# Kernel optimization log

Measured on AMD Instinct MI355X. Metric: run time of the kernel, lower is better.

Reference implementation:

```python
import jax, jax.numpy as jnp
import numpy as np

B, CIN, COUT, K = 4096, 128, 128, 9  # batch, in_ch, out_ch, board size / n_offsets


def setup_inputs() -> dict:
    key = jax.random.key(0)
    k1, k2, k3 = jax.random.split(key, 3)
    inputs = jax.random.normal(k1, (B, CIN, K, K), dtype=jnp.float32)   # [B, Cin, 9, 9]
    weights = jax.random.normal(k2, (K, COUT, CIN), dtype=jnp.float32)  # per-offset linear
    bias = jax.random.normal(k3, (K, COUT), dtype=jnp.float32)
    return {"inputs": inputs, "weights": weights, "bias": bias}


def reference(inputs, weights, bias):
    # For each vertical offset k (row of the 9x9 board), gather the slice
    # inputs[:, :, k, :] and apply the k-th linear map plus its bias.
    # out[b, k, oc, x] = sum_i W[k, oc, i] * inputs[b, i, k, x] + bias[k, oc]
    out = jnp.einsum('bikx,koi->bkox', inputs, weights)  # [B, 9, Cout, 9]
    out = out + bias[None, :, :, None]
    return out
```

## Files before the change

kernel.cpp:

```cpp
#include <hip/hip_runtime.h>
#include <hip/hip_bf16.h>


#define NB    4096
#define CINC  128
#define COUTC 128
#define NK    9
#define NX    9
#define BT    4
#define NCOL  (BT * NX)
#define LDK   136
#define ROWF  (NK * NX)
#define OUTK  (COUTC * NX)
#define OUTB  (NK * OUTK)
#define NWELT (NK * COUTC * CINC)

typedef __attribute__((ext_vector_type(8))) short short8;
typedef __attribute__((ext_vector_type(4))) float floatx4;

struct F4 { float x, y, z, w; };

__device__ __forceinline__ short f2bf(float f) {
    union { float f; unsigned u; } v; v.f = f;
    unsigned r = v.u + 0x7fff + ((v.u >> 16) & 1);
    return (short)(r >> 16);
}

__global__ __launch_bounds__(256) void GatherVertical_40656160424516_wconv(
    const float* __restrict__ w, short* __restrict__ wbf)
{
    int idx = blockIdx.x * 256 + threadIdx.x;
    wbf[idx] = f2bf(w[idx]);
}

__global__ __launch_bounds__(512, 8) void GatherVertical_40656160424516_kernel(
    const float* __restrict__ in, const short* __restrict__ wbf,
    const float* __restrict__ bias, float* __restrict__ out)
{
    __shared__ __align__(16) char smem[NCOL * LDK * 2 + BT * OUTK * 4];
    short* Il = (short*)smem;
    float* Ol = (float*)(smem + NCOL * LDK * 2);

    const int t = threadIdx.x;
    const int b0 = blockIdx.x * BT;

    const int lane = t & 63;
    const int wv = t >> 6;
    const int lc = lane & 15;
    const int quad = lane >> 4;
    const int oc_base = wv * 16;

    const int i_st = t & 127;
    const int bl_st = t >> 7;
    const float* rowp = in + ((size_t)(b0 + bl_st) * CINC + i_st) * ROWF;

    F4 sa, sb; float sc;
    auto issue_in = [&](int k) {
        const float* p = rowp + k * NX;
        sa = *(const F4*)p; sb = *(const F4*)(p + 4); sc = p[8];
    };
    issue_in(0);

    short* Ilb = Il + bl_st * (NX * LDK) + i_st;

    for (int k = 0; k < NK; ++k) {
        Ilb[0 * LDK] = f2bf(sa.x);
        Ilb[1 * LDK] = f2bf(sa.y);
        Ilb[2 * LDK] = f2bf(sa.z);
        Ilb[3 * LDK] = f2bf(sa.w);
        Ilb[4 * LDK] = f2bf(sb.x);
        Ilb[5 * LDK] = f2bf(sb.y);
        Ilb[6 * LDK] = f2bf(sb.z);
        Ilb[7 * LDK] = f2bf(sb.w);
        Ilb[8 * LDK] = f2bf(sc);

        asm volatile("s_waitcnt lgkmcnt(0)" ::: "memory");
        __builtin_amdgcn_s_barrier();

        const short* wpk = wbf + k * (COUTC * CINC) + (oc_base + lc) * CINC + quad * 8;
        short8 afr[4];
        #pragma unroll
        for (int s = 0; s < 4; ++s) afr[s] = *(const short8*)(wpk + s * 32);
        float4 bv = *(const float4*)(bias + k * COUTC + oc_base + quad * 4);
        __builtin_amdgcn_sched_barrier(0);
        if (k < NK - 1) issue_in(k + 1);
        __builtin_amdgcn_sched_barrier(0);

        float bsv[4] = {bv.x, bv.y, bv.z, bv.w};

        floatx4 acc[3];
        #pragma unroll
        for (int n = 0; n < 3; ++n) acc[n] = (floatx4){0.f, 0.f, 0.f, 0.f};
        #pragma unroll
        for (int s = 0; s < 4; ++s) {
            const int kof = s * 32 + quad * 8;
            #pragma unroll
            for (int n = 0; n < 3; ++n) {
                const int col = (n < 2) ? (n * 16 + lc) : (32 + (lc & 3));
                short8 bfr = *(const short8*)&Il[col * LDK + kof];
                acc[n] = __builtin_amdgcn_mfma_f32_16x16x32_bf16(afr[s], bfr, acc[n], 0, 0, 0);
            }
        }

        #pragma unroll
        for (int n = 0; n < 2; ++n) {
            int nx = n * 16 + lc;
            int bl = nx / 9;
            int x = nx - bl * 9;
            float* op = Ol + (bl * COUTC + oc_base + quad * 4) * NX + x;
            #pragma unroll
            for (int r = 0; r < 4; ++r) op[r * NX] = acc[n][r] + bsv[r];
        }
        if (lc < 4) {
            float* op = Ol + (3 * COUTC + oc_base + quad * 4) * NX + 5 + lc;
            #pragma unroll
            for (int r = 0; r < 4; ++r) op[r * NX] = acc[2][r] + bsv[r];
        }

        asm volatile("s_waitcnt lgkmcnt(0)" ::: "memory");
        __builtin_amdgcn_s_barrier();

        float* dstk = out + (size_t)b0 * OUTB + k * OUTK;
        #pragma unroll
        for (int c = 0; c < 2; ++c) {
            int fo = (c * 512 + t) * 4;
            int bl = fo / 1152;
            int rem = fo - bl * 1152;
            floatx4 v = *(const floatx4*)(Ol + fo);
            *(floatx4*)(dstk + (size_t)bl * OUTB + rem) = v;
        }
        if (t < 128) {
            int fo = (1024 + t) * 4;
            int rem = fo - 3 * 1152;
            floatx4 v = *(const floatx4*)(Ol + fo);
            *(floatx4*)(dstk + (size_t)3 * OUTB + rem) = v;
        }
    }
}

__global__ __launch_bounds__(512, 4) void GatherVertical_40656160424516_fb(
    const float* __restrict__ in, const float* __restrict__ w,
    const float* __restrict__ bias, float* __restrict__ out)
{
    __shared__ __align__(16) char smem[NCOL * LDK * 2 + BT * OUTK * 4];
    short* Il = (short*)smem;
    float* Ol = (float*)(smem + NCOL * LDK * 2);

    const int t = threadIdx.x;
    const int b0 = blockIdx.x * BT;
    const int lane = t & 63;
    const int wv = t >> 6;
    const int lc = lane & 15;
    const int quad = lane >> 4;
    const int oc_base = wv * 16;

    const int i_st = t & 127;
    const int bl_st = t >> 7;
    const float* rowp = in + ((size_t)(b0 + bl_st) * CINC + i_st) * ROWF;

    F4 sa, sb; float sc;
    auto issue_in = [&](int k) {
        const float* p = rowp + k * NX;
        sa = *(const F4*)p; sb = *(const F4*)(p + 4); sc = p[8];
    };
    issue_in(0);
    short* Ilb = Il + bl_st * (NX * LDK) + i_st;

    for (int k = 0; k < NK; ++k) {
        Ilb[0 * LDK] = f2bf(sa.x); Ilb[1 * LDK] = f2bf(sa.y);
        Ilb[2 * LDK] = f2bf(sa.z); Ilb[3 * LDK] = f2bf(sa.w);
        Ilb[4 * LDK] = f2bf(sb.x); Ilb[5 * LDK] = f2bf(sb.y);
        Ilb[6 * LDK] = f2bf(sb.z); Ilb[7 * LDK] = f2bf(sb.w);
        Ilb[8 * LDK] = f2bf(sc);

        asm volatile("s_waitcnt lgkmcnt(0)" ::: "memory");
        __builtin_amdgcn_s_barrier();

        const float* wp = w + k * (COUTC * CINC) + (oc_base + lc) * CINC + quad * 8;
        float4 w0[4], w1[4];
        #pragma unroll
        for (int s = 0; s < 4; ++s) {
            w0[s] = *(const float4*)(wp + s * 32);
            w1[s] = *(const float4*)(wp + s * 32 + 4);
        }
        float4 bv = *(const float4*)(bias + k * COUTC + oc_base + quad * 4);
        __builtin_amdgcn_sched_barrier(0);
        if (k < NK - 1) issue_in(k + 1);
        __builtin_amdgcn_sched_barrier(0);

        short8 afr[4];
        #pragma unroll
        for (int s = 0; s < 4; ++s) {
            short8 a;
            a[0] = f2bf(w0[s].x); a[1] = f2bf(w0[s].y);
            a[2] = f2bf(w0[s].z); a[3] = f2bf(w0[s].w);
            a[4] = f2bf(w1[s].x); a[5] = f2bf(w1[s].y);
            a[6] = f2bf(w1[s].z); a[7] = f2bf(w1[s].w);
            afr[s] = a;
        }
        float bsv[4] = {bv.x, bv.y, bv.z, bv.w};

        floatx4 acc[3];
        #pragma unroll
        for (int n = 0; n < 3; ++n) acc[n] = (floatx4){0.f, 0.f, 0.f, 0.f};
        #pragma unroll
        for (int s = 0; s < 4; ++s) {
            const int kof = s * 32 + quad * 8;
            #pragma unroll
            for (int n = 0; n < 3; ++n) {
                const int col = (n < 2) ? (n * 16 + lc) : (32 + (lc & 3));
                short8 bfr = *(const short8*)&Il[col * LDK + kof];
                acc[n] = __builtin_amdgcn_mfma_f32_16x16x32_bf16(afr[s], bfr, acc[n], 0, 0, 0);
            }
        }

        #pragma unroll
        for (int n = 0; n < 2; ++n) {
            int nx = n * 16 + lc;
            int bl = nx / 9;
            int x = nx - bl * 9;
            float* op = Ol + (bl * COUTC + oc_base + quad * 4) * NX + x;
            #pragma unroll
            for (int r = 0; r < 4; ++r) op[r * NX] = acc[n][r] + bsv[r];
        }
        if (lc < 4) {
            float* op = Ol + (3 * COUTC + oc_base + quad * 4) * NX + 5 + lc;
            #pragma unroll
            for (int r = 0; r < 4; ++r) op[r * NX] = acc[2][r] + bsv[r];
        }

        asm volatile("s_waitcnt lgkmcnt(0)" ::: "memory");
        __builtin_amdgcn_s_barrier();

        float* dstk = out + (size_t)b0 * OUTB + k * OUTK;
        #pragma unroll
        for (int c = 0; c < 2; ++c) {
            int fo = (c * 512 + t) * 4;
            int bl = fo / 1152;
            int rem = fo - bl * 1152;
            floatx4 v = *(const floatx4*)(Ol + fo);
            *(floatx4*)(dstk + (size_t)bl * OUTB + rem) = v;
        }
        if (t < 128) {
            int fo = (1024 + t) * 4;
            int rem = fo - 3 * 1152;
            floatx4 v = *(const floatx4*)(Ol + fo);
            *(floatx4*)(dstk + (size_t)3 * OUTB + rem) = v;
        }
    }
}

extern "C" void kernel_launch(void* const* d_in, const int* in_sizes, int n_in,
                              void* d_out, int out_size, void* d_ws, size_t ws_size,
                              hipStream_t stream) {
    const float* in  = (const float*)d_in[0];
    const float* w   = (const float*)d_in[1];
    const float* bs  = (const float*)d_in[2];
    float* out = (float*)d_out;
    const size_t WBF_BYTES = (size_t)NWELT * sizeof(short);
    if (d_ws != nullptr && ws_size >= WBF_BYTES) {
        short* wbf = (short*)d_ws;
        GatherVertical_40656160424516_wconv<<<NWELT / 256, 256, 0, stream>>>(w, wbf);
        GatherVertical_40656160424516_kernel<<<NB / BT, 512, 0, stream>>>(in, wbf, bs, out);
    } else {
        GatherVertical_40656160424516_fb<<<NB / BT, 512, 0, stream>>>(in, w, bs, out);
    }
}
```

Baseline: 374.2 us.

## Stage full input rows into LDS once per block with two-batch tiles

Instead of loading one 9-wide row slice per k iteration with register prefetch, each block now loads the whole contiguous 81-float row per channel for two batches into LDS up front using wide vector loads. The batch tile drops from four to two, so the MFMA N dimension shrinks to 18 columns (two 16-wide tiles with padding) and the grid doubles. The write-back and barrier layout are adjusted to match. The change trades per-k load/compute overlap for more coalesced input reads, and raises LDS use per batch, which lowers occupancy.

Result: faster. 351.3 us (-6.1%).

```diff
diff --git a/kernel.cpp b/kernel.cpp
--- a/kernel.cpp
+++ b/kernel.cpp
@@ -7,10 +7,10 @@
 #define COUTC 128
 #define NK    9
 #define NX    9
-#define BT    4
-#define NCOL  (BT * NX)
+#define BT    2
+#define ROWF  (NK * NX)
 #define LDK   136
-#define ROWF  (NK * NX)
+#define KSTR  (18 * LDK)
 #define OUTK  (COUTC * NX)
 #define OUTB  (NK * OUTK)
 #define NWELT (NK * COUTC * CINC)
@@ -24,6 +24,24 @@
     union { float f; unsigned u; } v; v.f = f;
     unsigned r = v.u + 0x7fff + ((v.u >> 16) & 1);
     return (short)(r >> 16);
+}
+
+__device__ __forceinline__ constexpr int koff(int kx) {
+    return (kx / 9) * KSTR + (kx % 9) * LDK;
+}
+
+template<int KX0>
+__device__ __forceinline__ void stage20(short* lb, const float* p) {
+    F4 v[5];
+    #pragma unroll
+    for (int c = 0; c < 5; ++c) v[c] = *(const F4*)(p + 4 * c);
+    #pragma unroll
+    for (int c = 0; c < 5; ++c) {
+        lb[koff(KX0 + 4 * c + 0)] = f2bf(v[c].x);
+        lb[koff(KX0 + 4 * c + 1)] = f2bf(v[c].y);
+        lb[koff(KX0 + 4 * c + 2)] = f2bf(v[c].z);
+        lb[koff(KX0 + 4 * c + 3)] = f2bf(v[c].w);
+    }
 }
 
 __global__ __launch_bounds__(256) void GatherVertical_40656160424516_wconv(
@@ -33,13 +51,13 @@
     wbf[idx] = f2bf(w[idx]);
 }
 
-__global__ __launch_bounds__(512, 8) void GatherVertical_40656160424516_kernel(
+__global__ __launch_bounds__(512, 6) void GatherVertical_40656160424516_kernel(
     const float* __restrict__ in, const short* __restrict__ wbf,
     const float* __restrict__ bias, float* __restrict__ out)
 {
-    __shared__ __align__(16) char smem[NCOL * LDK * 2 + BT * OUTK * 4];
+    __shared__ __align__(16) char smem[9 * KSTR * 2 + BT * OUTK * 4];
     short* Il = (short*)smem;
-    float* Ol = (float*)(smem + NCOL * LDK * 2);
+    float* Ol = (float*)(smem + 9 * KSTR * 2);
 
     const int t = threadIdx.x;
     const int b0 = blockIdx.x * BT;
@@ -50,90 +68,75 @@
     const int quad = lane >> 4;
     const int oc_base = wv * 16;
 
-    const int i_st = t & 127;
-    const int bl_st = t >> 7;
-    const float* rowp = in + ((size_t)(b0 + bl_st) * CINC + i_st) * ROWF;
-
-    F4 sa, sb; float sc;
-    auto issue_in = [&](int k) {
-        const float* p = rowp + k * NX;
-        sa = *(const F4*)p; sb = *(const F4*)(p + 4); sc = p[8];
-    };
-    issue_in(0);
-
-    short* Ilb = Il + bl_st * (NX * LDK) + i_st;
+    {
+        const int r = t & 255;
+        const int h = t >> 8;
+        const int bb = r >> 7;
+        const int i = r & 127;
+        const float* rowp = in + ((size_t)(b0 + bb) * CINC + i) * ROWF + 40 * h;
+        short* lb = Il + bb * (NX * LDK) + i;
+        if (h == 0) {
+            stage20<0>(lb, rowp);
+            stage20<20>(lb, rowp + 20);
+        } else {
+            stage20<40>(lb, rowp);
+            stage20<60>(lb, rowp + 20);
+            lb[koff(80)] = f2bf(rowp[40]);
+        }
+    }
+
+    asm volatile("s_waitcnt lgkmcnt(0)" ::: "memory");
+    __builtin_amdgcn_s_barrier();
 
     for (int k = 0; k < NK; ++k) {
-        Ilb[0 * LDK] = f2bf(sa.x);
-        Ilb[1 * LDK] = f2bf(sa.y);
-        Ilb[2 * LDK] = f2bf(sa.z);
-        Ilb[3 * LDK] = f2bf(sa.w);
-        Ilb[4 * LDK] = f2bf(sb.x);
-        Ilb[5 * LDK] = f2bf(sb.y);
-        Ilb[6 * LDK] = f2bf(sb.z);
-        Ilb[7 * LDK] = f2bf(sb.w);
-        Ilb[8 * LDK] = f2bf(sc);
-
-        asm volatile("s_waitcnt lgkmcnt(0)" ::: "memory");
-        __builtin_amdgcn_s_barrier();
-
         const short* wpk = wbf + k * (COUTC * CINC) + (oc_base + lc) * CINC + quad * 8;
         short8 afr[4];
         #pragma unroll
         for (int s = 0; s < 4; ++s) afr[s] = *(const short8*)(wpk + s * 32);
         float4 bv = *(const float4*)(bias + k * COUTC + oc_base + quad * 4);
-        __builtin_amdgcn_sched_barrier(0);
-        if (k < NK - 1) issue_in(k + 1);
-        __builtin_amdgcn_sched_barrier(0);
-
         float bsv[4] = {bv.x, bv.y, bv.z, bv.w};
 
-        floatx4 acc[3];
-        #pragma unroll
-        for (int n = 0; n < 3; ++n) acc[n] = (floatx4){0.f, 0.f, 0.f, 0.f};
-        #pragma unroll
-        for (int s = 0; s < 4; ++s) {
-            const int kof = s * 32 + quad * 8;
-            #pragma unroll
-            for (int n = 0; n < 3; ++n) {
-                const int col = (n < 2) ? (n * 16 + lc) : (32 + (lc & 3));
-                short8 bfr = *(const short8*)&Il[col * LDK + kof];
-                acc[n] = __builtin_amdgcn_mfma_f32_16x16x32_bf16(afr[s], bfr, acc[n], 0, 0, 0);
+        floatx4 acc0 = {0.f, 0.f, 0.f, 0.f};
+        floatx4 acc1 = {0.f, 0.f, 0.f, 0.f};
+        const short* bp = Il + k * KSTR + lc * LDK + quad * 8;
+        #pragma unroll
+        for (int s = 0; s < 4; ++s) {
+            short8 bf0 = *(const short8*)(bp + s * 32);
+            short8 bf1 = *(const short8*)(bp + 16 * LDK + s * 32);
+            acc0 = __builtin_amdgcn_mfma_f32_16x16x32_bf16(afr[s], bf0, acc0, 0, 0, 0);
+            acc1 = __builtin_amdgcn_mfma_f32_16x16x32_bf16(afr[s], bf1, acc1, 0, 0, 0);
+        }
+
+        asm volatile("s_waitcnt lgkmcnt(0)" ::: "memory");
+        __builtin_amdgcn_s_barrier();
+
+        {
+            int bcp = lc >= 9;
+            int x = lc - bcp * 9;
+            float* op = Ol + (bcp * COUTC + oc_base + quad * 4) * NX + x;
+            #pragma unroll
+            for (int rr = 0; rr < 4; ++rr) op[rr * NX] = acc0[rr] + bsv[rr];
+            if (lc < 2) {
+                float* op1 = Ol + (COUTC + oc_base + quad * 4) * NX + 7 + lc;
+                #pragma unroll
+                for (int rr = 0; rr < 4; ++rr) op1[rr * NX] = acc1[rr] + bsv[rr];
             }
         }
 
-        #pragma unroll
-        for (int n = 0; n < 2; ++n) {
-            int nx = n * 16 + lc;
-            int bl = nx / 9;
-            int x = nx - bl * 9;
-            float* op = Ol + (bl * COUTC + oc_base + quad * 4) * NX + x;
-            #pragma unroll
-            for (int r = 0; r < 4; ++r) op[r * NX] = acc[n][r] + bsv[r];
-        }
-        if (lc < 4) {
-            float* op = Ol + (3 * COUTC + oc_base + quad * 4) * NX + 5 + lc;
-            #pragma unroll
-            for (int r = 0; r < 4; ++r) op[r * NX] = acc[2][r] + bsv[r];
-        }
-
-        asm volatile("s_waitcnt lgkmcnt(0)" ::: "memory");
-        __builtin_amdgcn_s_barrier();
-
-        float* dstk = out + (size_t)b0 * OUTB + k * OUTK;
-        #pragma unroll
-        for (int c = 0; c < 2; ++c) {
-            int fo = (c * 512 + t) * 4;
-            int bl = fo / 1152;
-            int rem = fo - bl * 1152;
-            floatx4 v = *(const floatx4*)(Ol + fo);
-            *(floatx4*)(dstk + (size_t)bl * OUTB + rem) = v;
-        }
-        if (t < 128) {
-            int fo = (1024 + t) * 4;
-            int rem = fo - 3 * 1152;
-            floatx4 v = *(const floatx4*)(Ol + fo);
-            *(floatx4*)(dstk + (size_t)3 * OUTB + rem) = v;
+        asm volatile("s_waitcnt lgkmcnt(0)" ::: "memory");
+        __builtin_amdgcn_s_barrier();
+
+        {
+            float* dstb = out + (size_t)b0 * OUTB + k * OUTK;
+            int bcp = t >= 288;
+            int off = (t - bcp * 288) * 4;
+            floatx4 v = *(const floatx4*)(Ol + bcp * OUTK + off);
+            *(floatx4*)(dstb + (size_t)bcp * OUTB + off) = v;
+            if (t < 64) {
+                int off2 = (224 + t) * 4;
+                floatx4 v2 = *(const floatx4*)(Ol + OUTK + off2);
+                *(floatx4*)(dstb + (size_t)OUTB + off2) = v2;
+            }
         }
     }
 }
@@ -142,12 +145,12 @@
     const float* __restrict__ in, const float* __restrict__ w,
     const float* __restrict__ bias, float* __restrict__ out)
 {
-    __shared__ __align__(16) char smem[NCOL * LDK * 2 + BT * OUTK * 4];
-    short* Il = (short*)smem;
-    float* Ol = (float*)(smem + NCOL * LDK * 2);
+    __shared__ __align__(16) char smem2[36 * LDK * 2 + 4 * OUTK * 4];
+    short* Il = (short*)smem2;
+    float* Ol = (float*)(smem2 + 36 * LDK * 2);
 
     const int t = threadIdx.x;
-    const int b0 = blockIdx.x * BT;
+    const int b0 = blockIdx.x * 4;
     const int lane = t & 63;
     const int wv = t >> 6;
     const int lc = lane & 15;
@@ -263,6 +266,6 @@
         GatherVertical_40656160424516_wconv<<<NWELT / 256, 256, 0, stream>>>(w, wbf);
         GatherVertical_40656160424516_kernel<<<NB / BT, 512, 0, stream>>>(in, wbf, bs, out);
     } else {
-        GatherVertical_40656160424516_fb<<<NB / BT, 512, 0, stream>>>(in, w, bs, out);
-    }
-}
+        GatherVertical_40656160424516_fb<<<NB / 4, 512, 0, stream>>>(in, w, bs, out);
+    }
+}
```
